# Performance work log

Measured on AMD Instinct MI355X. Metric: run time of the kernel, lower is better.

The kernel has to match this reference:

```python
import jax, jax.numpy as jnp
import numpy as np

B, N, TOP_K, NUM_RBF, VNUM = 2, 2048, 30, 16, 2

def _normalize(v, axis=-1, eps=1e-8):
    return v / jnp.maximum(jnp.linalg.norm(v, axis=axis, keepdims=True), eps)

def _gather_nodes(nodes, idx):
    # nodes [B,N,C], idx [B,N,K] -> [B,N,K,C]
    return jnp.take_along_axis(nodes[:, :, None, :], idx[..., None], axis=1)

def _rbf(D):
    mu = jnp.linspace(0.0, 20.0, NUM_RBF)
    sigma = 20.0 / NUM_RBF
    return jnp.exp(-(((D[..., None] - mu) / sigma) ** 2))

def _rbf_node(A, C):
    return _rbf(jnp.sqrt(jnp.sum((A - C) ** 2, -1) + 1e-6))

def _rbf_edge(A, C, E_idx):
    Cn = _gather_nodes(C, E_idx)  # [B,N,K,3]
    return _rbf(jnp.sqrt(jnp.sum((A[:, :, None, :] - Cn) ** 2, -1) + 1e-6))

def _full_dist(Xc, mask, top_k, eps=1e-6):
    m2 = mask[:, None, :] * mask[:, :, None]
    dX = Xc[:, None, :, :] - Xc[:, :, None, :]
    D = (1.0 - m2) * 10000.0 + m2 * jnp.sqrt(jnp.sum(dX ** 2, -1) + eps)
    D_adj = D + (1.0 - m2) * (jnp.max(D, -1, keepdims=True) + 1.0)
    negv, idx = jax.lax.top_k(-D_adj, min(top_k, D_adj.shape[-1]))
    return -negv, idx

def _dihedrals(X, eps=1e-7):
    b, n = X.shape[:2]
    X3 = X[:, :, :3, :].reshape(b, 3 * n, 3)  # N,Ca,C backbone chain
    U = _normalize(X3[:, 1:, :] - X3[:, :-1, :])
    u0, u1, u2 = U[:, :-2, :], U[:, 1:-1, :], U[:, 2:, :]
    n0 = _normalize(jnp.cross(u0, u1))
    n1 = _normalize(jnp.cross(u1, u2))
    cosD = jnp.clip(jnp.sum(n0 * n1, -1), -1 + eps, 1 - eps)
    v = _normalize(jnp.cross(n0, n1))
    D = jnp.sign(jnp.sum(-v * u1, -1)) * jnp.arccos(cosD)
    D = jnp.pad(D, ((0, 0), (1, 2))).reshape(b, n, 3)
    dihed = jnp.concatenate([jnp.cos(D), jnp.sin(D)], -1)
    cosA = jnp.clip(jnp.sum(u0 * u1, -1), -1 + eps, 1 - eps)
    A = jnp.pad(jnp.arccos(cosA), ((0, 0), (1, 2))).reshape(b, n, 3)
    ang = jnp.concatenate([jnp.cos(A), jnp.sin(A)], -1)
    return jnp.concatenate([dihed, ang], -1)  # [B,N,12]

def _quaternions(R):
    Rxx, Ryy, Rzz = R[..., 0, 0], R[..., 1, 1], R[..., 2, 2]
    mags = 0.5 * jnp.sqrt(jnp.abs(1.0 + jnp.stack([Rxx - Ryy - Rzz, -Rxx + Ryy - Rzz, -Rxx - Ryy + Rzz], -1)))
    signs = jnp.sign(jnp.stack([R[..., 2, 1] - R[..., 1, 2], R[..., 0, 2] - R[..., 2, 0], R[..., 1, 0] - R[..., 0, 1]], -1))
    w = jnp.sqrt(jax.nn.relu(1.0 + Rxx + Ryy + Rzz))[..., None] / 2.0
    return _normalize(jnp.concatenate([signs * mags, w], -1))

def _orientations(X, E_idx):
    b, n = X.shape[:2]
    X3 = X[:, :, :3, :].reshape(b, 3 * n, 3)
    U = _normalize(X3[:, 1:, :] - X3[:, :-1, :])
    u0, u1 = U[:, :-2, :], U[:, 1:-1, :]
    n0 = _normalize(jnp.cross(u0, u1))[:, ::3, :]   # [B,N-1,3]
    b1 = _normalize(u0 - u1)[:, ::3, :]
    Xn = X3[:, ::3, :]                               # backbone N atoms [B,N,3]
    Q = jnp.stack((b1, n0, jnp.cross(b1, n0)), 2).reshape(b, n - 1, 9)
    Q = jnp.pad(Q, ((0, 0), (0, 1), (0, 0)))         # [B,N,9]
    Q3 = Q.reshape(b, n, 3, 3)
    Qn = _gather_nodes(Q, E_idx).reshape(b, n, -1, 3, 3)
    nb = [_gather_nodes(X[:, :, i, :], E_idx) for i in (1, 0, 2, 3)]  # Ca,N,C,O neighbors
    dXn = jnp.stack(nb, 3) - Xn[:, :, None, None, :]  # [B,N,K,4,3]
    dU = jnp.einsum('bnij,bnkaj->bnkai', Q3, dXn)
    E_direct = _normalize(dU).reshape(b, n, -1, 12)
    R = jnp.einsum('bnji,bnkjl->bnkil', Q3, Qn)
    q = _quaternions(R)                               # [B,N,K,4]
    dX_inner = X[:, :, jnp.array([0, 2, 3]), :] - Xn[:, :, None, :]
    dU_inner = _normalize(jnp.einsum('bnij,bnaj->bnai', Q3, dX_inner))
    V_direct = dU_inner.reshape(b, n, 9)
    return V_direct, E_direct, q

NODE_PAIRS = [('Ca','N'),('Ca','C'),('Ca','O'),('N','C'),('N','O'),('O','C'),('Ca','Cb'),('Cb','N'),('Cb','O'),('C','Cb')]
EDGE_PAIRS = [('Ca','Ca'),('Ca','C'),('C','Ca'),('Ca','N'),('N','Ca'),('Cb','Ca'),('Ca','Cb'),('Cb','N'),('N','Cb'),('Cb','O'),('O','Cb'),('Cb','C'),('C','Cb'),('Cb','Cb'),('Ca','O'),('O','Ca'),('C','C'),('C','N'),('N','C'),('C','O'),('O','C'),('N','N'),('N','O'),('O','N'),('O','O')]

def _forward(X, mask, virtual_atoms):
    Xca = X[:, :, 1, :]
    D_neighbors, E_idx = _full_dist(Xca, mask, TOP_K)
    V_angles = _dihedrals(X)
    V_direct, E_direct, E_angles = _orientations(X, E_idx)
    aN, aCa, aC, aO = X[:, :, 0, :], X[:, :, 1, :], X[:, :, 2, :], X[:, :, 3, :]
    bv = aCa - aN
    cv = aC - aCa
    av = jnp.cross(bv, cv)
    aCb = -0.58273431 * av + 0.56802827 * bv - 0.54067466 * cv + aCa
    atoms = {'N': aN, 'Ca': aCa, 'C': aC, 'O': aO, 'Cb': aCb}
    va = virtual_atoms / jnp.linalg.norm(virtual_atoms, axis=1, keepdims=True)
    vat = [va[i, 0] * av + va[i, 1] * bv + va[i, 2] * cv + aCa for i in range(VNUM)]
    node_dist = [_rbf_node(atoms[a1], atoms[a2]) for a1, a2 in NODE_PAIRS]
    for i in range(VNUM):
        for j in range(i):
            node_dist.append(_rbf_node(vat[i], vat[j]))
            node_dist.append(_rbf_node(vat[j], vat[i]))
    V_dist = jnp.concatenate(node_dist, -1)  # [B,N,12*16]
    edge_dist = [_rbf_edge(atoms[a1], atoms[a2], E_idx) for a1, a2 in EDGE_PAIRS]
    for i in range(VNUM):
        edge_dist.append(_rbf_edge(vat[i], vat[i], E_idx))
    # faithfully replicate source: the cross-virtual j-loop is dedented and only runs for the final i
    i = VNUM - 1
    for j in range(i):
        edge_dist.append(_rbf_edge(vat[i], vat[j], E_idx))
        edge_dist.append(_rbf_edge(vat[j], vat[i], E_idx))
    E_dist = jnp.concatenate(edge_dist, -1)  # [B,N,K,29*16]
    V = jnp.concatenate([V_dist, V_angles, V_direct], -1)   # [B,N,213]
    E = jnp.concatenate([E_dist, E_angles, E_direct], -1)   # [B,N,K,480]
    return V, E, E_idx

def setup_inputs():
    key = jax.random.key(0)
    k1, k2 = jax.random.split(key)
    X = jax.random.normal(k1, (B, N, 4, 3), dtype=jnp.float32)
    mask = jnp.ones((B, N), dtype=jnp.float32)
    virtual_atoms = jax.random.normal(k2, (VNUM, 3), dtype=jnp.float32)
    return {"X": X, "mask": mask, "virtual_atoms": virtual_atoms}

def reference(X, mask, virtual_atoms):
    return _forward(X, mask, virtual_atoms)
```

## Files before the change

kernel.cpp:

```cpp
#include <hip/hip_runtime.h>
#include <math.h>

#define BB 2
#define NN 2048
#define KK 30
#define NRBF 16
#define V_DIM 213
#define E_DIM 480
#define NODES (BB*NN)
#define PREPB 64
#define NPP 64

typedef unsigned long long u64;
typedef unsigned int u32;
typedef float v4f __attribute__((ext_vector_type(4)));

__device__ __forceinline__ float sgnf(float x){ return (x>0.f)?1.f:((x<0.f)?-1.f:0.f); }

__device__ __forceinline__ void cross3(const float* a, const float* b, float* c){
  c[0]=a[1]*b[2]-a[2]*b[1];
  c[1]=a[2]*b[0]-a[0]*b[2];
  c[2]=a[0]*b[1]-a[1]*b[0];
}
__device__ __forceinline__ void norm3e(float* v){
  float n = sqrtf(v[0]*v[0]+v[1]*v[1]+v[2]*v[2]);
  float inv = 1.0f/fmaxf(n,1e-8f);
  v[0]*=inv; v[1]*=inv; v[2]*=inv;
}
__device__ __forceinline__ float dot3(const float* a, const float* b){
  return a[0]*b[0]+a[1]*b[1]+a[2]*b[2];
}

__device__ __forceinline__ void node_derived(const float* p, const float (*va)[3],
                                             float* full, int isLast){
  for(int i=0;i<12;i++) full[i]=p[i];
  float bv[3],cv[3],av[3];
  for(int c=0;c<3;c++){ bv[c]=p[3+c]-p[c]; cv[c]=p[6+c]-p[3+c]; }
  cross3(bv,cv,av);
  for(int c=0;c<3;c++)
    full[12+c] = -0.58273431f*av[c] + 0.56802827f*bv[c] - 0.54067466f*cv[c] + p[3+c];
  for(int i=0;i<2;i++)
    for(int c=0;c<3;c++)
      full[15+3*i+c] = va[i][0]*av[c] + va[i][1]*bv[c] + va[i][2]*cv[c] + p[3+c];
  if (isLast){
    for(int i=0;i<9;i++) full[21+i]=0.f;
  } else {
    float u0[3],u1[3];
    for(int c=0;c<3;c++){ u0[c]=bv[c]; u1[c]=cv[c]; }
    norm3e(u0); norm3e(u1);
    float n0[3]; cross3(u0,u1,n0); norm3e(n0);
    float b1[3]; for(int c=0;c<3;c++) b1[c]=u0[c]-u1[c];
    norm3e(b1);
    float c2[3]; cross3(b1,n0,c2);
    for(int c=0;c<3;c++){ full[21+c]=b1[c]; full[24+c]=n0[c]; full[27+c]=c2[c]; }
  }
}

__device__ __constant__ int c_epA[29] = {1,1,2,1,0,4,1,4,0,4,3,4,2,4,1,3,2,2,0,2,3,0,0,3,3, 5,6,6,5};
__device__ __constant__ int c_epB[29] = {1,2,1,0,1,1,4,0,4,3,4,2,4,4,3,1,2,0,2,3,2,0,3,0,3, 5,6,5,6};
__device__ __constant__ int c_npA[12] = {1,1,1,0,0,3,1,4,4,2,6,5};
__device__ __constant__ int c_npB[12] = {0,2,3,2,3,2,4,0,3,4,5,6};

#define NBIN 2048
#define BINSHIFT 21

__global__ __launch_bounds__(256) void topk_prep_kernel(const float* __restrict__ X,
                                                        const float* __restrict__ mask,
                                                        const float* __restrict__ vatoms,
                                                        float* __restrict__ outIdx,
                                                        float* __restrict__ outV,
                                                        float* __restrict__ packets){
  __shared__ __align__(16) char smem[24576];
  __shared__ float wred[4];
  __shared__ u32 wsum[4];
  __shared__ int s_cutbin;
  __shared__ u32 s_m;

  const int t = threadIdx.x;

  if (blockIdx.x < PREPB){
    float* pk_s   = (float*)smem;
    float* dist_s = (float*)(smem + NPP*32*4);
    float* tail_s = (float*)(smem + NPP*32*4 + NPP*12*4);
    const int node0 = blockIdx.x * NPP;

    if (t < NPP){
      const int node = node0 + t;
      const int b = node/NN, n = node%NN;

      float va[2][3];
      for(int i=0;i<2;i++){
        float x=vatoms[3*i],y=vatoms[3*i+1],z=vatoms[3*i+2];
        float inv=1.f/sqrtf(x*x+y*y+z*z);
        va[i][0]=x*inv; va[i][1]=y*inv; va[i][2]=z*inv;
      }
      float p[12];
      { const float* q = X + (size_t)node*12; for(int i=0;i<12;i++) p[i]=q[i]; }
      float full[30];
      node_derived(p, va, full, n==NN-1);

      float* pk = pk_s + t*32;
      for (int i=0;i<30;i++) pk[i]=full[i];
      pk[30]=0.f; pk[31]=0.f;

      for (int blk=0; blk<12; blk++){
        const float* a=&full[3*c_npA[blk]];
        const float* c=&full[3*c_npB[blk]];
        float dx=a[0]-c[0], dy=a[1]-c[1], dz=a[2]-c[2];
        dist_s[t*12+blk] = sqrtf(dx*dx+dy*dy+dz*dz+1e-6f);
      }

      float P[6][3];
      for (int o=0;o<6;o++){
        int m = 3*n-1+o;
        if (m>=0 && m<3*NN){
          int res=m/3, at=m-3*res;
          const float* qq = X + ((size_t)b*NN+res)*12 + at*3;
          P[o][0]=qq[0]; P[o][1]=qq[1]; P[o][2]=qq[2];
        } else { P[o][0]=P[o][1]=P[o][2]=0.f; }
      }
      float U[5][3];
      for (int o=0;o<5;o++){
        for(int c=0;c<3;c++) U[o][c]=P[o+1][c]-P[o][c];
        norm3e(U[o]);
      }
      float Dv[3], Av[3];
      for (int r=0;r<3;r++){
        int i3 = 3*n + r;
        if (i3>=1 && i3<=3*NN-3){
          float* u0=U[r]; float* u1=U[r+1]; float* u2=U[r+2];
          float n0[3],n1[3];
          cross3(u0,u1,n0); norm3e(n0);
          cross3(u1,u2,n1); norm3e(n1);
          float cosD = fminf(fmaxf(dot3(n0,n1), -1.f+1e-7f), 1.f-1e-7f);
          float v[3]; cross3(n0,n1,v); norm3e(v);
          float s = -(v[0]*u1[0]+v[1]*u1[1]+v[2]*u1[2]);
          Dv[r] = sgnf(s)*acosf(cosD);
          float cosA = fminf(fmaxf(dot3(u0,u1), -1.f+1e-7f), 1.f-1e-7f);
          Av[r] = acosf(cosA);
        } else { Dv[r]=0.f; Av[r]=0.f; }
      }
      float* tl = tail_s + t*21;
      for (int r=0;r<3;r++){
        tl[0+r]=cosf(Dv[r]);
        tl[3+r]=sinf(Dv[r]);
        tl[6+r]=cosf(Av[r]);
        tl[9+r]=sinf(Av[r]);
      }
      const int aord[3]={0,2,3};
      for (int a2=0;a2<3;a2++){
        int a=aord[a2];
        float d[3]; for(int c=0;c<3;c++) d[c]=full[3*a+c]-full[c];
        float dU[3];
        for(int i=0;i<3;i++)
          dU[i]=full[21+3*i]*d[0]+full[21+3*i+1]*d[1]+full[21+3*i+2]*d[2];
        norm3e(dU);
        for(int c=0;c<3;c++) tl[12+3*a2+c]=dU[c];
      }
    }
    __syncthreads();

    float* vbase = outV + (size_t)node0*V_DIM;
    for (int g=t; g<NPP*V_DIM; g+=256){
      int node=g/V_DIM, f=g-V_DIM*node;
      float val;
      if (f < 192){
        float D = dist_s[node*12 + (f>>4)];
        float t2 = (D - (20.0f/15.0f)*(float)(f&15))*0.8f;
        val = __expf(-t2*t2);
      } else {
        val = tail_s[node*21 + (f-192)];
      }
      vbase[g]=val;
    }
    v4f* pdst = (v4f*)(packets + (size_t)node0*32);
    const v4f* psrc = (const v4f*)pk_s;
    for (int g=t; g<NPP*8; g+=256) pdst[g]=psrc[g];
    return;
  }

  u32* bins = (u32*)smem;
  u64* cand = (u64*)(smem + NBIN*4);

  const int row = blockIdx.x - PREPB;
  const int b = row / NN, n = row % NN;
  const int w = t>>6, l = t&63;

  for (int i=t;i<NBIN;i+=256) bins[i]=0;
  if (t==0) s_m=0;

  const float* Xb = X + (size_t)b*NN*12;
  const float* mb = mask + (size_t)b*NN;
  const float cx=Xb[n*12+3], cy=Xb[n*12+4], cz=Xb[n*12+5], mn=mb[n];

  float dval[8];
  float lmax = -1e30f;
  #pragma unroll
  for (int s=0;s<8;s++){
    int i = s*256+t;
    const float* p = Xb + i*12;
    float dx=__fsub_rn(p[3],cx), dy=__fsub_rn(p[4],cy), dz=__fsub_rn(p[5],cz);
    float ss=__fadd_rn(__fadd_rn(__fadd_rn(__fmul_rn(dx,dx),__fmul_rn(dy,dy)),
                                 __fmul_rn(dz,dz)), 1e-6f);
    float d = __fsqrt_rn(ss);
    float m2 = __fmul_rn(mb[i], mn);
    float om = __fsub_rn(1.0f, m2);
    float D  = __fadd_rn(__fmul_rn(om,10000.0f), __fmul_rn(m2,d));
    dval[s]=D;
    lmax = fmaxf(lmax, D);
  }
  #pragma unroll
  for (int off=32; off; off>>=1) lmax = fmaxf(lmax, __shfl_xor(lmax, off));
  if (l==0) wred[w]=lmax;
  __syncthreads();
  const float srmax = fmaxf(fmaxf(wred[0],wred[1]), fmaxf(wred[2],wred[3]));
  const float radd = __fadd_rn(srmax, 1.0f);

  u32 keyb[8];
  #pragma unroll
  for (int s=0;s<8;s++){
    int i = s*256+t;
    float m2 = __fmul_rn(mb[i], mn);
    float om = __fsub_rn(1.0f, m2);
    float Dj = __fadd_rn(dval[s], __fmul_rn(om, radd));
    u32 kb = __float_as_uint(Dj);
    keyb[s]=kb;
    u32 bin = kb >> BINSHIFT;
    atomicAdd(&bins[(bin&7)*256 + (bin>>3)], 1u);
  }
  __syncthreads();

  u32 g8[8]; u32 lsum=0;
  #pragma unroll
  for (int j=0;j<8;j++){ g8[j]=bins[j*256+t]; lsum+=g8[j]; }
  u32 inc=lsum;
  #pragma unroll
  for (int off=1; off<64; off<<=1){
    u32 o = __shfl_up(inc, off);
    if (l >= off) inc += o;
  }
  if (l==63) wsum[w]=inc;
  __syncthreads();
  u32 waveoff=0;
  for (int ww=0; ww<w; ww++) waveoff += wsum[ww];
  u32 run = waveoff + inc - lsum;
  #pragma unroll
  for (int j=0;j<8;j++){
    u32 c=g8[j];
    if (run < KK && run + c >= KK) s_cutbin = 8*t+j;
    run += c;
  }
  __syncthreads();
  const int cutbin = s_cutbin;

  #pragma unroll
  for (int s=0;s<8;s++){
    if ((int)(keyb[s] >> BINSHIFT) <= cutbin){
      u32 slot = atomicAdd(&s_m, 1u);
      cand[slot] = ((u64)keyb[s] << 32) | (u32)(s*256+t);
    }
  }
  __syncthreads();
  const int m = (int)s_m;

  for (int cix=t; cix<m; cix+=256){
    u64 mykey = cand[cix];
    int rank=0;
    for (int j=0;j<m;j++) rank += (cand[j] < mykey) ? 1 : 0;
    if (rank < KK)
      outIdx[(size_t)row*KK + rank] = (float)(u32)(mykey & 0xffffffffu);
  }
}

__device__ __forceinline__ void edge_tail_quat(const float* own, const float* nbk, float* tl){
  float R[3][3];
  for(int i=0;i<3;i++)for(int l2=0;l2<3;l2++){
    float s=0.f;
    for(int j=0;j<3;j++) s += own[21+3*j+i]*nbk[21+3*j+l2];
    R[i][l2]=s;
  }
  float Rxx=R[0][0],Ryy=R[1][1],Rzz=R[2][2];
  float m0=0.5f*sqrtf(fabsf(1.f+Rxx-Ryy-Rzz));
  float m1=0.5f*sqrtf(fabsf(1.f-Rxx+Ryy-Rzz));
  float m2=0.5f*sqrtf(fabsf(1.f-Rxx-Ryy+Rzz));
  float qx=sgnf(R[2][1]-R[1][2])*m0;
  float qy=sgnf(R[0][2]-R[2][0])*m1;
  float qz=sgnf(R[1][0]-R[0][1])*m2;
  float w =0.5f*sqrtf(fmaxf(1.f+Rxx+Ryy+Rzz,0.f));
  float inv=1.f/fmaxf(sqrtf(qx*qx+qy*qy+qz*qz+w*w),1e-8f);
  tl[0]=qx*inv; tl[1]=qy*inv; tl[2]=qz*inv; tl[3]=w*inv;
}

__global__ __launch_bounds__(256) void edge_kernel(const float* __restrict__ packets,
                                                   const float* __restrict__ outIdx,
                                                   float* __restrict__ outE){
  __shared__ __align__(16) float own[32];
  __shared__ __align__(16) float nb[KK][32];
  __shared__ int   jarr[KK];
  __shared__ float dist[KK*29];
  __shared__ __align__(16) float tail[KK][16];

  const int tid = threadIdx.x;
  const int row = blockIdx.x;
  const int b = row/NN;

  if (tid<KK) jarr[tid] = (int)outIdx[(size_t)row*KK+tid];
  if (tid>=248){
    int c = tid-248;
    ((v4f*)own)[c] = ((const v4f*)(packets + (size_t)row*32))[c];
  }
  __syncthreads();

  if (tid < 240){
    int k = tid>>3, c = tid&7;
    ((v4f*)&nb[k][0])[c] =
      ((const v4f*)(packets + ((size_t)b*NN + jarr[k])*32))[c];
  }
  __syncthreads();

  for (int g=tid; g<KK*29; g+=256){
    int k=g/29, c=g-29*k;
    const float* a  = &own[3*c_epA[c]];
    const float* bq = &nb[k][3*c_epB[c]];
    float dx=a[0]-bq[0], dy=a[1]-bq[1], dz=a[2]-bq[2];
    dist[g] = sqrtf(dx*dx+dy*dy+dz*dz+1e-6f);
  }

  if (tid < KK){
    edge_tail_quat(own, &nb[tid][0], &tail[tid][0]);
  } else if (tid >= 64 && tid < 64+KK*4){
    const int it = tid-64;
    const int k = it>>2, a2 = it&3;
    const int aord[4]={1,0,2,3};
    int a=aord[a2];
    float d[3]; for(int c=0;c<3;c++) d[c]=nb[k][3*a+c]-own[c];
    float dU[3];
    for(int i=0;i<3;i++)
      dU[i]=own[21+3*i]*d[0]+own[21+3*i+1]*d[1]+own[21+3*i+2]*d[2];
    norm3e(dU);
    tail[k][4+3*a2+0]=dU[0]; tail[k][4+3*a2+1]=dU[1]; tail[k][4+3*a2+2]=dU[2];
  }
  __syncthreads();

  v4f* eb = reinterpret_cast<v4f*>(outE + (size_t)row*KK*E_DIM);
  for (int g=tid; g<KK*120; g+=256){
    int k=g/120, q=g-120*k;
    v4f v;
    if (q < 116){
      float d = dist[k*29 + (q>>2)];
      float r0 = (float)((q&3)*4);
      float t0 = (d - (20.0f/15.0f)*(r0+0.f))*0.8f;
      float t1 = (d - (20.0f/15.0f)*(r0+1.f))*0.8f;
      float t2 = (d - (20.0f/15.0f)*(r0+2.f))*0.8f;
      float t3 = (d - (20.0f/15.0f)*(r0+3.f))*0.8f;
      v.x=__expf(-t0*t0); v.y=__expf(-t1*t1); v.z=__expf(-t2*t2); v.w=__expf(-t3*t3);
    } else {
      const float* tl = &tail[k][(q-116)*4];
      v.x=tl[0]; v.y=tl[1]; v.z=tl[2]; v.w=tl[3];
    }
    __builtin_nontemporal_store(v, &eb[g]);
  }
}

extern "C" void kernel_launch(void* const* d_in, const int* in_sizes, int n_in,
                              void* d_out, int out_size, void* d_ws, size_t ws_size,
                              hipStream_t stream) {
  (void)in_sizes; (void)n_in; (void)out_size; (void)ws_size;
  const float* X    = (const float*)d_in[0];
  const float* mask = (const float*)d_in[1];
  const float* vat  = (const float*)d_in[2];
  float* out = (float*)d_out;

  float* outV   = out;
  float* outE   = out + (size_t)NODES*V_DIM;
  float* outIdx = out + (size_t)NODES*V_DIM + (size_t)NODES*KK*E_DIM;
  float* packets = (float*)d_ws;

  hipLaunchKernelGGL(topk_prep_kernel, dim3(PREPB + NODES), dim3(256), 0, stream,
                     X, mask, vat, outIdx, outV, packets);
  hipLaunchKernelGGL(edge_kernel, dim3(NODES), dim3(256), 0, stream,
                     packets, outIdx, outE);
}
```

Baseline: 279.3 us.

## Fuse top-k, node features and edge features into one per-row kernel

Merges the top-k/prep kernel and the edge kernel into one kernel with one block per row. Each block computes its own top-k, then recomputes the derived node frames for itself and its 30 neighbours directly from X instead of reading a precomputed packet buffer. This removes the second launch, the packet round-trip through global memory and the reload of the indices. In exchange, node_derived is computed redundantly (about 31 times per node), and the serial per-thread prep work sits on the critical path of every block.

New measurement: 269.1 us. 3.7% less time.

```diff
diff --git a/kernel.cpp b/kernel.cpp
--- a/kernel.cpp
+++ b/kernel.cpp
@@ -8,8 +8,6 @@
 #define V_DIM 213
 #define E_DIM 480
 #define NODES (BB*NN)
-#define PREPB 64
-#define NPP 64
 
 typedef unsigned long long u64;
 typedef unsigned int u32;
@@ -64,214 +62,6 @@
 #define NBIN 2048
 #define BINSHIFT 21
 
-__global__ __launch_bounds__(256) void topk_prep_kernel(const float* __restrict__ X,
-                                                        const float* __restrict__ mask,
-                                                        const float* __restrict__ vatoms,
-                                                        float* __restrict__ outIdx,
-                                                        float* __restrict__ outV,
-                                                        float* __restrict__ packets){
-  __shared__ __align__(16) char smem[24576];
-  __shared__ float wred[4];
-  __shared__ u32 wsum[4];
-  __shared__ int s_cutbin;
-  __shared__ u32 s_m;
-
-  const int t = threadIdx.x;
-
-  if (blockIdx.x < PREPB){
-    float* pk_s   = (float*)smem;
-    float* dist_s = (float*)(smem + NPP*32*4);
-    float* tail_s = (float*)(smem + NPP*32*4 + NPP*12*4);
-    const int node0 = blockIdx.x * NPP;
-
-    if (t < NPP){
-      const int node = node0 + t;
-      const int b = node/NN, n = node%NN;
-
-      float va[2][3];
-      for(int i=0;i<2;i++){
-        float x=vatoms[3*i],y=vatoms[3*i+1],z=vatoms[3*i+2];
-        float inv=1.f/sqrtf(x*x+y*y+z*z);
-        va[i][0]=x*inv; va[i][1]=y*inv; va[i][2]=z*inv;
-      }
-      float p[12];
-      { const float* q = X + (size_t)node*12; for(int i=0;i<12;i++) p[i]=q[i]; }
-      float full[30];
-      node_derived(p, va, full, n==NN-1);
-
-      float* pk = pk_s + t*32;
-      for (int i=0;i<30;i++) pk[i]=full[i];
-      pk[30]=0.f; pk[31]=0.f;
-
-      for (int blk=0; blk<12; blk++){
-        const float* a=&full[3*c_npA[blk]];
-        const float* c=&full[3*c_npB[blk]];
-        float dx=a[0]-c[0], dy=a[1]-c[1], dz=a[2]-c[2];
-        dist_s[t*12+blk] = sqrtf(dx*dx+dy*dy+dz*dz+1e-6f);
-      }
-
-      float P[6][3];
-      for (int o=0;o<6;o++){
-        int m = 3*n-1+o;
-        if (m>=0 && m<3*NN){
-          int res=m/3, at=m-3*res;
-          const float* qq = X + ((size_t)b*NN+res)*12 + at*3;
-          P[o][0]=qq[0]; P[o][1]=qq[1]; P[o][2]=qq[2];
-        } else { P[o][0]=P[o][1]=P[o][2]=0.f; }
-      }
-      float U[5][3];
-      for (int o=0;o<5;o++){
-        for(int c=0;c<3;c++) U[o][c]=P[o+1][c]-P[o][c];
-        norm3e(U[o]);
-      }
-      float Dv[3], Av[3];
-      for (int r=0;r<3;r++){
-        int i3 = 3*n + r;
-        if (i3>=1 && i3<=3*NN-3){
-          float* u0=U[r]; float* u1=U[r+1]; float* u2=U[r+2];
-          float n0[3],n1[3];
-          cross3(u0,u1,n0); norm3e(n0);
-          cross3(u1,u2,n1); norm3e(n1);
-          float cosD = fminf(fmaxf(dot3(n0,n1), -1.f+1e-7f), 1.f-1e-7f);
-          float v[3]; cross3(n0,n1,v); norm3e(v);
-          float s = -(v[0]*u1[0]+v[1]*u1[1]+v[2]*u1[2]);
-          Dv[r] = sgnf(s)*acosf(cosD);
-          float cosA = fminf(fmaxf(dot3(u0,u1), -1.f+1e-7f), 1.f-1e-7f);
-          Av[r] = acosf(cosA);
-        } else { Dv[r]=0.f; Av[r]=0.f; }
-      }
-      float* tl = tail_s + t*21;
-      for (int r=0;r<3;r++){
-        tl[0+r]=cosf(Dv[r]);
-        tl[3+r]=sinf(Dv[r]);
-        tl[6+r]=cosf(Av[r]);
-        tl[9+r]=sinf(Av[r]);
-      }
-      const int aord[3]={0,2,3};
-      for (int a2=0;a2<3;a2++){
-        int a=aord[a2];
-        float d[3]; for(int c=0;c<3;c++) d[c]=full[3*a+c]-full[c];
-        float dU[3];
-        for(int i=0;i<3;i++)
-          dU[i]=full[21+3*i]*d[0]+full[21+3*i+1]*d[1]+full[21+3*i+2]*d[2];
-        norm3e(dU);
-        for(int c=0;c<3;c++) tl[12+3*a2+c]=dU[c];
-      }
-    }
-    __syncthreads();
-
-    float* vbase = outV + (size_t)node0*V_DIM;
-    for (int g=t; g<NPP*V_DIM; g+=256){
-      int node=g/V_DIM, f=g-V_DIM*node;
-      float val;
-      if (f < 192){
-        float D = dist_s[node*12 + (f>>4)];
-        float t2 = (D - (20.0f/15.0f)*(float)(f&15))*0.8f;
-        val = __expf(-t2*t2);
-      } else {
-        val = tail_s[node*21 + (f-192)];
-      }
-      vbase[g]=val;
-    }
-    v4f* pdst = (v4f*)(packets + (size_t)node0*32);
-    const v4f* psrc = (const v4f*)pk_s;
-    for (int g=t; g<NPP*8; g+=256) pdst[g]=psrc[g];
-    return;
-  }
-
-  u32* bins = (u32*)smem;
-  u64* cand = (u64*)(smem + NBIN*4);
-
-  const int row = blockIdx.x - PREPB;
-  const int b = row / NN, n = row % NN;
-  const int w = t>>6, l = t&63;
-
-  for (int i=t;i<NBIN;i+=256) bins[i]=0;
-  if (t==0) s_m=0;
-
-  const float* Xb = X + (size_t)b*NN*12;
-  const float* mb = mask + (size_t)b*NN;
-  const float cx=Xb[n*12+3], cy=Xb[n*12+4], cz=Xb[n*12+5], mn=mb[n];
-
-  float dval[8];
-  float lmax = -1e30f;
-  #pragma unroll
-  for (int s=0;s<8;s++){
-    int i = s*256+t;
-    const float* p = Xb + i*12;
-    float dx=__fsub_rn(p[3],cx), dy=__fsub_rn(p[4],cy), dz=__fsub_rn(p[5],cz);
-    float ss=__fadd_rn(__fadd_rn(__fadd_rn(__fmul_rn(dx,dx),__fmul_rn(dy,dy)),
-                                 __fmul_rn(dz,dz)), 1e-6f);
-    float d = __fsqrt_rn(ss);
-    float m2 = __fmul_rn(mb[i], mn);
-    float om = __fsub_rn(1.0f, m2);
-    float D  = __fadd_rn(__fmul_rn(om,10000.0f), __fmul_rn(m2,d));
-    dval[s]=D;
-    lmax = fmaxf(lmax, D);
-  }
-  #pragma unroll
-  for (int off=32; off; off>>=1) lmax = fmaxf(lmax, __shfl_xor(lmax, off));
-  if (l==0) wred[w]=lmax;
-  __syncthreads();
-  const float srmax = fmaxf(fmaxf(wred[0],wred[1]), fmaxf(wred[2],wred[3]));
-  const float radd = __fadd_rn(srmax, 1.0f);
-
-  u32 keyb[8];
-  #pragma unroll
-  for (int s=0;s<8;s++){
-    int i = s*256+t;
-    float m2 = __fmul_rn(mb[i], mn);
-    float om = __fsub_rn(1.0f, m2);
-    float Dj = __fadd_rn(dval[s], __fmul_rn(om, radd));
-    u32 kb = __float_as_uint(Dj);
-    keyb[s]=kb;
-    u32 bin = kb >> BINSHIFT;
-    atomicAdd(&bins[(bin&7)*256 + (bin>>3)], 1u);
-  }
-  __syncthreads();
-
-  u32 g8[8]; u32 lsum=0;
-  #pragma unroll
-  for (int j=0;j<8;j++){ g8[j]=bins[j*256+t]; lsum+=g8[j]; }
-  u32 inc=lsum;
-  #pragma unroll
-  for (int off=1; off<64; off<<=1){
-    u32 o = __shfl_up(inc, off);
-    if (l >= off) inc += o;
-  }
-  if (l==63) wsum[w]=inc;
-  __syncthreads();
-  u32 waveoff=0;
-  for (int ww=0; ww<w; ww++) waveoff += wsum[ww];
-  u32 run = waveoff + inc - lsum;
-  #pragma unroll
-  for (int j=0;j<8;j++){
-    u32 c=g8[j];
-    if (run < KK && run + c >= KK) s_cutbin = 8*t+j;
-    run += c;
-  }
-  __syncthreads();
-  const int cutbin = s_cutbin;
-
-  #pragma unroll
-  for (int s=0;s<8;s++){
-    if ((int)(keyb[s] >> BINSHIFT) <= cutbin){
-      u32 slot = atomicAdd(&s_m, 1u);
-      cand[slot] = ((u64)keyb[s] << 32) | (u32)(s*256+t);
-    }
-  }
-  __syncthreads();
-  const int m = (int)s_m;
-
-  for (int cix=t; cix<m; cix+=256){
-    u64 mykey = cand[cix];
-    int rank=0;
-    for (int j=0;j<m;j++) rank += (cand[j] < mykey) ? 1 : 0;
-    if (rank < KK)
-      outIdx[(size_t)row*KK + rank] = (float)(u32)(mykey & 0xffffffffu);
-  }
-}
-
 __device__ __forceinline__ void edge_tail_quat(const float* own, const float* nbk, float* tl){
   float R[3][3];
   for(int i=0;i<3;i++)for(int l2=0;l2<3;l2++){
@@ -291,63 +81,236 @@
   tl[0]=qx*inv; tl[1]=qy*inv; tl[2]=qz*inv; tl[3]=w*inv;
 }
 
-__global__ __launch_bounds__(256) void edge_kernel(const float* __restrict__ packets,
-                                                   const float* __restrict__ outIdx,
-                                                   float* __restrict__ outE){
-  __shared__ __align__(16) float own[32];
-  __shared__ __align__(16) float nb[KK][32];
-  __shared__ int   jarr[KK];
-  __shared__ float dist[KK*29];
-  __shared__ __align__(16) float tail[KK][16];
-
-  const int tid = threadIdx.x;
+__global__ __launch_bounds__(256) void fused_kernel(const float* __restrict__ X,
+                                                    const float* __restrict__ mask,
+                                                    const float* __restrict__ vatoms,
+                                                    float* __restrict__ outIdx,
+                                                    float* __restrict__ outV,
+                                                    float* __restrict__ outE){
+  __shared__ __align__(16) char smem[24576];
+  __shared__ float wred[4];
+  __shared__ u32 wsum[4];
+  __shared__ int s_cutbin;
+  __shared__ u32 s_m;
+  __shared__ int jarr[KK];
+
+  const int t = threadIdx.x;
   const int row = blockIdx.x;
-  const int b = row/NN;
-
-  if (tid<KK) jarr[tid] = (int)outIdx[(size_t)row*KK+tid];
-  if (tid>=248){
-    int c = tid-248;
-    ((v4f*)own)[c] = ((const v4f*)(packets + (size_t)row*32))[c];
-  }
-  __syncthreads();
-
-  if (tid < 240){
-    int k = tid>>3, c = tid&7;
-    ((v4f*)&nb[k][0])[c] =
-      ((const v4f*)(packets + ((size_t)b*NN + jarr[k])*32))[c];
-  }
-  __syncthreads();
-
-  for (int g=tid; g<KK*29; g+=256){
-    int k=g/29, c=g-29*k;
-    const float* a  = &own[3*c_epA[c]];
-    const float* bq = &nb[k][3*c_epB[c]];
-    float dx=a[0]-bq[0], dy=a[1]-bq[1], dz=a[2]-bq[2];
-    dist[g] = sqrtf(dx*dx+dy*dy+dz*dz+1e-6f);
-  }
-
-  if (tid < KK){
-    edge_tail_quat(own, &nb[tid][0], &tail[tid][0]);
-  } else if (tid >= 64 && tid < 64+KK*4){
-    const int it = tid-64;
-    const int k = it>>2, a2 = it&3;
-    const int aord[4]={1,0,2,3};
+  const int b = row / NN, n = row % NN;
+  const int w = t>>6, l = t&63;
+
+  u32* bins = (u32*)smem;
+  u64* cand = (u64*)(smem + NBIN*4);
+
+  for (int i=t;i<NBIN;i+=256) bins[i]=0;
+  if (t==0) s_m=0;
+
+  const float* Xb = X + (size_t)b*NN*12;
+  const float* mb = mask + (size_t)b*NN;
+  const float cx=Xb[n*12+3], cy=Xb[n*12+4], cz=Xb[n*12+5], mn=mb[n];
+
+  float dval[8], m2v[8];
+  float lmax = -1e30f;
+  #pragma unroll
+  for (int s=0;s<8;s++){
+    int i = s*256+t;
+    const float* p = Xb + i*12;
+    float dx=__fsub_rn(p[3],cx), dy=__fsub_rn(p[4],cy), dz=__fsub_rn(p[5],cz);
+    float ss=__fadd_rn(__fadd_rn(__fadd_rn(__fmul_rn(dx,dx),__fmul_rn(dy,dy)),
+                                 __fmul_rn(dz,dz)), 1e-6f);
+    float d = __fsqrt_rn(ss);
+    float m2 = __fmul_rn(mb[i], mn);
+    m2v[s]=m2;
+    float om = __fsub_rn(1.0f, m2);
+    float D  = __fadd_rn(__fmul_rn(om,10000.0f), __fmul_rn(m2,d));
+    dval[s]=D;
+    lmax = fmaxf(lmax, D);
+  }
+  #pragma unroll
+  for (int off=32; off; off>>=1) lmax = fmaxf(lmax, __shfl_xor(lmax, off));
+  if (l==0) wred[w]=lmax;
+  __syncthreads();
+  const float srmax = fmaxf(fmaxf(wred[0],wred[1]), fmaxf(wred[2],wred[3]));
+  const float radd = __fadd_rn(srmax, 1.0f);
+
+  u32 keyb[8];
+  #pragma unroll
+  for (int s=0;s<8;s++){
+    float m2 = m2v[s];
+    float om = __fsub_rn(1.0f, m2);
+    float Dj = __fadd_rn(dval[s], __fmul_rn(om, radd));
+    u32 kb = __float_as_uint(Dj);
+    keyb[s]=kb;
+    u32 bin = kb >> BINSHIFT;
+    atomicAdd(&bins[(bin&7)*256 + (bin>>3)], 1u);
+  }
+  __syncthreads();
+
+  u32 g8[8]; u32 lsum=0;
+  #pragma unroll
+  for (int j=0;j<8;j++){ g8[j]=bins[j*256+t]; lsum+=g8[j]; }
+  u32 inc=lsum;
+  #pragma unroll
+  for (int off=1; off<64; off<<=1){
+    u32 o = __shfl_up(inc, off);
+    if (l >= off) inc += o;
+  }
+  if (l==63) wsum[w]=inc;
+  __syncthreads();
+  u32 waveoff=0;
+  for (int ww=0; ww<w; ww++) waveoff += wsum[ww];
+  u32 run = waveoff + inc - lsum;
+  #pragma unroll
+  for (int j=0;j<8;j++){
+    u32 c=g8[j];
+    if (run < KK && run + c >= KK) s_cutbin = 8*t+j;
+    run += c;
+  }
+  __syncthreads();
+  const int cutbin = s_cutbin;
+
+  #pragma unroll
+  for (int s=0;s<8;s++){
+    if ((int)(keyb[s] >> BINSHIFT) <= cutbin){
+      u32 slot = atomicAdd(&s_m, 1u);
+      cand[slot] = ((u64)keyb[s] << 32) | (u32)(s*256+t);
+    }
+  }
+  __syncthreads();
+  const int m = (int)s_m;
+
+  for (int cix=t; cix<m; cix+=256){
+    u64 mykey = cand[cix];
+    int rank=0;
+    for (int j=0;j<m;j++) rank += (cand[j] < mykey) ? 1 : 0;
+    if (rank < KK){
+      int idx = (int)(u32)(mykey & 0xffffffffu);
+      outIdx[(size_t)row*KK + rank] = (float)idx;
+      jarr[rank] = idx;
+    }
+  }
+  __syncthreads();
+
+  float* own   = (float*)smem;
+  float* nbp   = own + 32;
+  float* edist = nbp + KK*32;
+  float* tailE = edist + 872;
+  float* dist_s= tailE + KK*16;
+  float* tail_s= dist_s + 12;
+
+  if (t < 31){
+    float va[2][3];
+    for(int i=0;i<2;i++){
+      float x=vatoms[3*i],y=vatoms[3*i+1],z=vatoms[3*i+2];
+      float inv=1.f/sqrtf(x*x+y*y+z*z);
+      va[i][0]=x*inv; va[i][1]=y*inv; va[i][2]=z*inv;
+    }
+    if (t < KK){
+      const int j = jarr[t];
+      float p[12];
+      { const float* q = Xb + (size_t)j*12; for(int i=0;i<12;i++) p[i]=q[i]; }
+      float full[30];
+      node_derived(p, va, full, j==NN-1);
+      for(int i=0;i<30;i++) nbp[t*32+i]=full[i];
+    } else {
+      float p[12];
+      { const float* q = Xb + (size_t)n*12; for(int i=0;i<12;i++) p[i]=q[i]; }
+      float full[30];
+      node_derived(p, va, full, n==NN-1);
+      for(int i=0;i<30;i++) own[i]=full[i];
+    }
+  } else if (t >= 31 && t < 34){
+    const int r = t-31;
+    float P[4][3];
+    for (int o=0;o<4;o++){
+      int mm = 3*n - 1 + r + o;
+      if (mm>=0 && mm<3*NN){
+        int res=mm/3, at=mm-3*res;
+        const float* qq = Xb + (size_t)res*12 + at*3;
+        P[o][0]=qq[0]; P[o][1]=qq[1]; P[o][2]=qq[2];
+      } else { P[o][0]=P[o][1]=P[o][2]=0.f; }
+    }
+    float U[3][3];
+    for (int o=0;o<3;o++){
+      for(int c=0;c<3;c++) U[o][c]=P[o+1][c]-P[o][c];
+      norm3e(U[o]);
+    }
+    float Dv=0.f, Av=0.f;
+    int i3 = 3*n + r;
+    if (i3>=1 && i3<=3*NN-3){
+      float n0[3],n1[3];
+      cross3(U[0],U[1],n0); norm3e(n0);
+      cross3(U[1],U[2],n1); norm3e(n1);
+      float cosD = fminf(fmaxf(dot3(n0,n1), -1.f+1e-7f), 1.f-1e-7f);
+      float v[3]; cross3(n0,n1,v); norm3e(v);
+      float s = -(v[0]*U[1][0]+v[1]*U[1][1]+v[2]*U[1][2]);
+      Dv = sgnf(s)*acosf(cosD);
+      float cosA = fminf(fmaxf(dot3(U[0],U[1]), -1.f+1e-7f), 1.f-1e-7f);
+      Av = acosf(cosA);
+    }
+    tail_s[0+r]=cosf(Dv); tail_s[3+r]=sinf(Dv);
+    tail_s[6+r]=cosf(Av); tail_s[9+r]=sinf(Av);
+  }
+  __syncthreads();
+
+  if (t < KK){
+    edge_tail_quat(own, &nbp[t*32], &tailE[t*16]);
+  }
+  if (t < 12){
+    const float* a=&own[3*c_npA[t]];
+    const float* c=&own[3*c_npB[t]];
+    float dx=a[0]-c[0], dy=a[1]-c[1], dz=a[2]-c[2];
+    dist_s[t] = sqrtf(dx*dx+dy*dy+dz*dz+1e-6f);
+  } else if (t < 15){
+    const int a2 = t-12;
+    const int aord[3]={0,2,3};
     int a=aord[a2];
-    float d[3]; for(int c=0;c<3;c++) d[c]=nb[k][3*a+c]-own[c];
+    float d[3]; for(int c=0;c<3;c++) d[c]=own[3*a+c]-own[c];
     float dU[3];
     for(int i=0;i<3;i++)
       dU[i]=own[21+3*i]*d[0]+own[21+3*i+1]*d[1]+own[21+3*i+2]*d[2];
     norm3e(dU);
-    tail[k][4+3*a2+0]=dU[0]; tail[k][4+3*a2+1]=dU[1]; tail[k][4+3*a2+2]=dU[2];
-  }
-  __syncthreads();
+    for(int c=0;c<3;c++) tail_s[12+3*a2+c]=dU[c];
+  } else if (t >= 64 && t < 64+KK*4){
+    const int it = t-64;
+    const int k = it>>2, a2 = it&3;
+    const int aord[4]={1,0,2,3};
+    int a=aord[a2];
+    float d[3]; for(int c=0;c<3;c++) d[c]=nbp[k*32+3*a+c]-own[c];
+    float dU[3];
+    for(int i=0;i<3;i++)
+      dU[i]=own[21+3*i]*d[0]+own[21+3*i+1]*d[1]+own[21+3*i+2]*d[2];
+    norm3e(dU);
+    tailE[k*16+4+3*a2+0]=dU[0]; tailE[k*16+4+3*a2+1]=dU[1]; tailE[k*16+4+3*a2+2]=dU[2];
+  }
+  for (int g=t; g<KK*29; g+=256){
+    int k=g/29, c=g-29*k;
+    const float* a  = &own[3*c_epA[c]];
+    const float* bq = &nbp[k*32+3*c_epB[c]];
+    float dx=a[0]-bq[0], dy=a[1]-bq[1], dz=a[2]-bq[2];
+    edist[g] = sqrtf(dx*dx+dy*dy+dz*dz+1e-6f);
+  }
+  __syncthreads();
+
+  float* vb = outV + (size_t)row*V_DIM;
+  for (int g=t; g<V_DIM; g+=256){
+    float val;
+    if (g < 192){
+      float D = dist_s[g>>4];
+      float t2 = (D - (20.0f/15.0f)*(float)(g&15))*0.8f;
+      val = __expf(-t2*t2);
+    } else {
+      val = tail_s[g-192];
+    }
+    vb[g]=val;
+  }
 
   v4f* eb = reinterpret_cast<v4f*>(outE + (size_t)row*KK*E_DIM);
-  for (int g=tid; g<KK*120; g+=256){
+  for (int g=t; g<KK*120; g+=256){
     int k=g/120, q=g-120*k;
     v4f v;
     if (q < 116){
-      float d = dist[k*29 + (q>>2)];
+      float d = edist[k*29 + (q>>2)];
       float r0 = (float)((q&3)*4);
       float t0 = (d - (20.0f/15.0f)*(r0+0.f))*0.8f;
       float t1 = (d - (20.0f/15.0f)*(r0+1.f))*0.8f;
@@ -355,7 +318,7 @@
       float t3 = (d - (20.0f/15.0f)*(r0+3.f))*0.8f;
       v.x=__expf(-t0*t0); v.y=__expf(-t1*t1); v.z=__expf(-t2*t2); v.w=__expf(-t3*t3);
     } else {
-      const float* tl = &tail[k][(q-116)*4];
+      const float* tl = &tailE[k*16 + (q-116)*4];
       v.x=tl[0]; v.y=tl[1]; v.z=tl[2]; v.w=tl[3];
     }
     __builtin_nontemporal_store(v, &eb[g]);
@@ -365,7 +328,7 @@
 extern "C" void kernel_launch(void* const* d_in, const int* in_sizes, int n_in,
                               void* d_out, int out_size, void* d_ws, size_t ws_size,
                               hipStream_t stream) {
-  (void)in_sizes; (void)n_in; (void)out_size; (void)ws_size;
+  (void)in_sizes; (void)n_in; (void)out_size; (void)d_ws; (void)ws_size;
   const float* X    = (const float*)d_in[0];
   const float* mask = (const float*)d_in[1];
   const float* vat  = (const float*)d_in[2];
@@ -374,10 +337,7 @@
   float* outV   = out;
   float* outE   = out + (size_t)NODES*V_DIM;
   float* outIdx = out + (size_t)NODES*V_DIM + (size_t)NODES*KK*E_DIM;
-  float* packets = (float*)d_ws;
-
-  hipLaunchKernelGGL(topk_prep_kernel, dim3(PREPB + NODES), dim3(256), 0, stream,
-                     X, mask, vat, outIdx, outV, packets);
-  hipLaunchKernelGGL(edge_kernel, dim3(NODES), dim3(256), 0, stream,
-                     packets, outIdx, outE);
-}
+
+  hipLaunchKernelGGL(fused_kernel, dim3(NODES), dim3(256), 0, stream,
+                     X, mask, vat, outIdx, outV, outE);
+}
```
